# Optimization experiments

Measured on AMD Instinct MI355X. Metric: run time of the kernel, lower is better.

Reference implementation:

```python
import jax, jax.numpy as jnp
import numpy as np

B, T, C, HEAD = 4, 4096, 1024, 64
SCALE = 1.0 / (C ** 0.5)  # module divides by embedding_size**0.5, not head_size**0.5


def setup_inputs() -> dict:
    key = jax.random.key(0)
    kx, kq, kk, kv = jax.random.split(key, 4)
    x = jax.random.normal(kx, (B, T, C), dtype=jnp.float32)
    # nn.Linear(C, head_size, bias=False) weights, stored as (C, head_size) for x @ W
    Wq = jax.random.normal(kq, (C, HEAD), dtype=jnp.float32) * (1.0 / np.sqrt(C))
    Wk = jax.random.normal(kk, (C, HEAD), dtype=jnp.float32) * (1.0 / np.sqrt(C))
    Wv = jax.random.normal(kv, (C, HEAD), dtype=jnp.float32) * (1.0 / np.sqrt(C))
    return {"x": x, "Wq": Wq, "Wk": Wk, "Wv": Wv}


def reference(x, Wq, Wk, Wv):
    q = jnp.einsum('btc,ch->bth', x, Wq)  # [B,T,HEAD]
    k = jnp.einsum('btc,ch->bth', x, Wk)
    v = jnp.einsum('btc,ch->bth', x, Wv)
    aff = jnp.einsum('bqh,bkh->bqk', q, k) * SCALE  # [B,T,T]
    causal = jnp.tril(jnp.ones((T, T), dtype=bool))
    aff = jnp.where(causal, aff, -jnp.inf)
    p = jax.nn.softmax(aff, axis=-1)  # dropout p=0.0 -> identity
    return jnp.einsum('bqk,bkh->bqh', p, v)  # [B,T,HEAD]
```

## Files before the change

kernel.cpp:

```cpp
#include <hip/hip_runtime.h>

#define T_SEQ 4096
#define NBATCH 4
#define CDIM 1024
#define NHEAD 64
#define SCALE (1.0f / 32.0f)
#define LOG2E 1.4426950408889634f
#define BT (NBATCH * T_SEQ)
#define NW 8
#define WREG 8960
#define THR2 11.0f

typedef __bf16 bf16x8 __attribute__((ext_vector_type(8)));
typedef float f32x4 __attribute__((ext_vector_type(4)));
typedef float f32x16 __attribute__((ext_vector_type(16)));
typedef unsigned long long u64;

__device__ __forceinline__ unsigned short f2bf(float f) {
  union { float f; unsigned u; } x;
  x.f = f;
  unsigned r = x.u + 0x7FFFu + ((x.u >> 16) & 1u);
  return (unsigned short)(r >> 16);
}

__device__ __forceinline__ unsigned cvt_pk(float lo, float hi) {
  unsigned d;
  asm("v_cvt_pk_bf16_f32 %0, %1, %2" : "=v"(d) : "v"(lo), "v"(hi));
  return d;
}

__device__ __forceinline__ f32x4 mfma16(bf16x8 a, bf16x8 b, f32x4 c) {
  return __builtin_amdgcn_mfma_f32_16x16x32_bf16(a, b, c, 0, 0, 0);
}

__device__ __forceinline__ f32x16 mfma32(bf16x8 a, bf16x8 b, f32x16 c) {
  return __builtin_amdgcn_mfma_f32_32x32x16_bf16(a, b, c, 0, 0, 0);
}

__global__ void prep_w(const float* __restrict__ Wq, const float* __restrict__ Wk,
                       const float* __restrict__ Wv, unsigned short* __restrict__ Wt) {
  int c = blockIdx.x;
  const float* W = (c < 64) ? Wq : (c < 128) ? Wk : Wv;
  int cc = c & 63;
  float sc = (c < 64) ? (SCALE * LOG2E) : 1.0f;
  for (int k = threadIdx.x; k < CDIM; k += blockDim.x)
    Wt[c * CDIM + k] = f2bf(W[k * NHEAD + cc] * sc);
}

__global__ __launch_bounds__(256) void proj_qkv(
    const float* __restrict__ x, const unsigned short* __restrict__ Wt,
    unsigned short* __restrict__ qws, unsigned short* __restrict__ kws,
    unsigned short* __restrict__ vtws) {
  __shared__ unsigned short xlds[32][136];
  const int tid = threadIdx.x;
  const int lane = tid & 63;
  const int w = tid >> 6;
  const int g = lane >> 4;
  const int c15 = lane & 15;
  const int rb = blockIdx.x * 32;

  f32x4 acc[2][3];
  for (int i = 0; i < 2; i++)
    for (int j = 0; j < 3; j++) acc[i][j] = (f32x4){0.f, 0.f, 0.f, 0.f};

  const int sr = tid >> 3;
  const int scc = (tid & 7) * 16;
  const float* xrow = x + (size_t)(rb + sr) * CDIM + scc;

  float4 cur[4];
  for (int i = 0; i < 4; i++) cur[i] = *(const float4*)(xrow + i * 4);

  for (int k0 = 0; k0 < CDIM; k0 += 128) {
    unsigned short pk[16];
    for (int i = 0; i < 4; i++) {
      pk[i * 4 + 0] = f2bf(cur[i].x);
      pk[i * 4 + 1] = f2bf(cur[i].y);
      pk[i * 4 + 2] = f2bf(cur[i].z);
      pk[i * 4 + 3] = f2bf(cur[i].w);
    }
    *(bf16x8*)&xlds[sr][scc] = *(bf16x8*)&pk[0];
    *(bf16x8*)&xlds[sr][scc + 8] = *(bf16x8*)&pk[8];
    __syncthreads();
    if (k0 + 128 < CDIM)
      for (int i = 0; i < 4; i++)
        cur[i] = *(const float4*)(xrow + k0 + 128 + i * 4);

    bf16x8 wfrag[4][3];
    for (int kk = 0; kk < 4; kk++)
      for (int bn = 0; bn < 3; bn++) {
        int col = w * 48 + bn * 16 + c15;
        wfrag[kk][bn] =
            *(const bf16x8*)&Wt[(size_t)col * CDIM + k0 + kk * 32 + g * 8];
      }

    for (int kk = 0; kk < 4; kk++) {
      bf16x8 a[2];
      for (int mt = 0; mt < 2; mt++)
        a[mt] = *(bf16x8*)&xlds[mt * 16 + c15][kk * 32 + g * 8];
      for (int bn = 0; bn < 3; bn++)
        for (int mt = 0; mt < 2; mt++)
          acc[mt][bn] = mfma16(a[mt], wfrag[kk][bn], acc[mt][bn]);
    }
    __syncthreads();
  }

  for (int mt = 0; mt < 2; mt++)
    for (int bn = 0; bn < 3; bn++) {
      int col = w * 48 + bn * 16 + c15;
      int row0 = rb + mt * 16 + 4 * g;
      for (int r = 0; r < 4; r++) {
        unsigned short v = f2bf(acc[mt][bn][r]);
        int t = row0 + r;
        if (col < 64)
          qws[(size_t)t * 64 + col] = v;
        else if (col < 128)
          kws[(size_t)t * 64 + (col - 64)] = v;
        else
          vtws[(size_t)(col - 128) * BT + t] = v;
      }
    }
}

__global__ __launch_bounds__(512, 2) void attn_fwd(
    const unsigned short* __restrict__ qws, const unsigned short* __restrict__ kws,
    const unsigned short* __restrict__ vtws, float* __restrict__ out) {
  __shared__ __align__(16) char smem[NW * WREG];
  const int tid = threadIdx.x;
  const int lane = tid & 63;
  const int w = tid >> 6;
  const int q31 = lane & 31;
  const int hi = lane >> 5;
  const int b = blockIdx.x >> 6;
  const int pi = blockIdx.x & 63;
  const size_t rowbase = (size_t)b * T_SEQ;
  char* wbase = smem + w * WREG;

  for (int half = 0; half < 2; ++half) {
    const int qt = half ? (127 - pi) : pi;
    const int qb = qt * 32;
    const int nsteps = qt + 1;

    bf16x8 qf[4];
    for (int h2 = 0; h2 < 4; h2++)
      qf[h2] = *(const bf16x8*)&qws[(rowbase + qb + q31) * 64 + h2 * 16 + hi * 8];

    f32x16 o[2];
    o[0] = (f32x16)0.f;
    o[1] = (f32x16)0.f;
    float mrow = -1e30f;
    float lrun = 0.f;

    for (int st = w; st < nsteps; st += NW) {
      const int kt = st * 32;
      bf16x8 ka[4];
      for (int h2 = 0; h2 < 4; h2++)
        ka[h2] =
            *(const bf16x8*)&kws[(rowbase + kt + q31) * 64 + h2 * 16 + hi * 8];
      bf16x8 va[2][2];
      for (int nt = 0; nt < 2; nt++)
        for (int ki = 0; ki < 2; ki++)
          va[nt][ki] = *(const bf16x8*)&vtws[(size_t)(nt * 32 + q31) * BT +
                                             rowbase + kt + ki * 16 + hi * 8];

      f32x16 s = (f32x16)0.f;
      for (int h2 = 0; h2 < 4; h2++) s = mfma32(ka[h2], qf[h2], s);

      float sv[16];
      for (int r = 0; r < 16; r++) sv[r] = s[r];

      if (st == nsteps - 1) {
        for (int r = 0; r < 16; r++) {
          int key = kt + (r & 3) + 8 * (r >> 2) + 4 * hi;
          if (key > qb + q31) sv[r] = -1e30f;
        }
      }

      float t01 = fmaxf(sv[0], sv[1]), t23 = fmaxf(sv[2], sv[3]);
      float t45 = fmaxf(sv[4], sv[5]), t67 = fmaxf(sv[6], sv[7]);
      float t89 = fmaxf(sv[8], sv[9]), tab = fmaxf(sv[10], sv[11]);
      float tcd = fmaxf(sv[12], sv[13]), tef = fmaxf(sv[14], sv[15]);
      float t = fmaxf(fmaxf(fmaxf(t01, t23), fmaxf(t45, t67)),
                      fmaxf(fmaxf(t89, tab), fmaxf(tcd, tef)));
      t = fmaxf(t, __shfl_xor(t, 32));
      if (__any(t > mrow + THR2)) {
        float mn = fmaxf(mrow, t);
        float a = exp2f(mrow - mn);
        mrow = mn;
        o[0] *= a;
        o[1] *= a;
        lrun *= a;
      }
      float p[16];
      for (int r = 0; r < 16; r++) p[r] = exp2f(sv[r] - mrow);

      float ssum = 0.f;
      for (int r = 0; r < 16; r++) ssum += p[r];
      lrun += ssum + __shfl_xor(ssum, 32);

      unsigned X[8], Y[8];
      for (int j = 0; j < 8; j++) X[j] = cvt_pk(p[2 * j], p[2 * j + 1]);
      for (int j = 0; j < 8; j++) Y[j] = __shfl_xor(X[j], 32);

      union { unsigned u[4]; bf16x8 v; } bf0, bf1;
      bf0.u[0] = hi ? Y[2] : X[0];
      bf0.u[1] = hi ? Y[3] : X[1];
      bf0.u[2] = hi ? X[2] : Y[0];
      bf0.u[3] = hi ? X[3] : Y[1];
      bf1.u[0] = hi ? Y[6] : X[4];
      bf1.u[1] = hi ? Y[7] : X[5];
      bf1.u[2] = hi ? X[6] : Y[4];
      bf1.u[3] = hi ? X[7] : Y[5];

      for (int nt = 0; nt < 2; nt++) {
        o[nt] = mfma32(va[nt][0], bf0.v, o[nt]);
        o[nt] = mfma32(va[nt][1], bf1.v, o[nt]);
      }
    }

    float* ow = (float*)wbase;
    float* mw = (float*)(wbase + 8704);
    float* lw = (float*)(wbase + 8832);
    for (int nt = 0; nt < 2; nt++)
      for (int r = 0; r < 16; r++) {
        int d = nt * 32 + (r & 3) + 8 * (r >> 2) + 4 * hi;
        ow[q31 * 68 + d] = o[nt][r];
      }
    if (hi == 0) {
      mw[q31] = mrow;
      lw[q31] = lrun;
    }
    __syncthreads();

    for (int i = 0; i < 4; i++) {
      int e = tid + i * 512;
      int row = e >> 6;
      int d = e & 63;
      float M = -1e30f;
      for (int ww = 0; ww < NW; ww++)
        M = fmaxf(M, ((const float*)(smem + ww * WREG + 8704))[row]);
      float L = 0.f, O = 0.f;
      for (int ww = 0; ww < NW; ww++) {
        float mv = ((const float*)(smem + ww * WREG + 8704))[row];
        float f = exp2f(mv - M);
        L += f * ((const float*)(smem + ww * WREG + 8832))[row];
        O += f * ((const float*)(smem + ww * WREG))[row * 68 + d];
      }
      out[(rowbase + qb + row) * 64 + d] = O / L;
    }
    __syncthreads();
  }
}

extern "C" void kernel_launch(void* const* d_in, const int* in_sizes, int n_in,
                              void* d_out, int out_size, void* d_ws, size_t ws_size,
                              hipStream_t stream) {
  const float* x = (const float*)d_in[0];
  const float* Wq = (const float*)d_in[1];
  const float* Wk = (const float*)d_in[2];
  const float* Wv = (const float*)d_in[3];
  float* out = (float*)d_out;

  char* ws = (char*)d_ws;
  unsigned short* Wt = (unsigned short*)(ws);
  unsigned short* qws = (unsigned short*)(ws + 393216);
  unsigned short* kws = (unsigned short*)(ws + 393216 + 2097152);
  unsigned short* vtws = (unsigned short*)(ws + 393216 + 2 * 2097152);

  prep_w<<<dim3(192), dim3(256), 0, stream>>>(Wq, Wk, Wv, Wt);
  proj_qkv<<<dim3(512), dim3(256), 0, stream>>>(x, Wt, qws, kws, vtws);
  attn_fwd<<<dim3(256), dim3(512), 0, stream>>>(qws, kws, vtws, out);
}
```

Measured before the change: 79.65 us.

## Double-buffer projection LDS, use permlane32 swap, drop lazy rescale

The QKV projection kernel gains a second LDS buffer, so the next x tile is converted and stored while the current one is consumed by MFMAs, which removes one barrier per k-step. In the attention loop, eight cross-half shuffles plus selects are replaced with four v_permlane32_swap instructions to build the P operand. The thresholded lazy max rescale is also dropped in favour of an unconditional rescale every step. That removes the wave-wide vote and branch, but adds an exp2 and multiplies of the O accumulators on every step.

```diff
diff --git a/kernel.cpp b/kernel.cpp
--- a/kernel.cpp
+++ b/kernel.cpp
@@ -9,12 +9,10 @@
 #define BT (NBATCH * T_SEQ)
 #define NW 8
 #define WREG 8960
-#define THR2 11.0f
 
 typedef __bf16 bf16x8 __attribute__((ext_vector_type(8)));
 typedef float f32x4 __attribute__((ext_vector_type(4)));
 typedef float f32x16 __attribute__((ext_vector_type(16)));
-typedef unsigned long long u64;
 
 __device__ __forceinline__ unsigned short f2bf(float f) {
   union { float f; unsigned u; } x;
@@ -27,6 +25,10 @@
   unsigned d;
   asm("v_cvt_pk_bf16_f32 %0, %1, %2" : "=v"(d) : "v"(lo), "v"(hi));
   return d;
+}
+
+__device__ __forceinline__ void swap32(unsigned& a, unsigned& b) {
+  asm("v_permlane32_swap_b32 %0, %1" : "+v"(a), "+v"(b));
 }
 
 __device__ __forceinline__ f32x4 mfma16(bf16x8 a, bf16x8 b, f32x4 c) {
@@ -51,7 +53,7 @@
     const float* __restrict__ x, const unsigned short* __restrict__ Wt,
     unsigned short* __restrict__ qws, unsigned short* __restrict__ kws,
     unsigned short* __restrict__ vtws) {
-  __shared__ unsigned short xlds[32][136];
+  __shared__ unsigned short xlds[2][32][136];
   const int tid = threadIdx.x;
   const int lane = tid & 63;
   const int w = tid >> 6;
@@ -67,10 +69,9 @@
   const int scc = (tid & 7) * 16;
   const float* xrow = x + (size_t)(rb + sr) * CDIM + scc;
 
-  float4 cur[4];
-  for (int i = 0; i < 4; i++) cur[i] = *(const float4*)(xrow + i * 4);
-
-  for (int k0 = 0; k0 < CDIM; k0 += 128) {
+  {
+    float4 cur[4];
+    for (int i = 0; i < 4; i++) cur[i] = *(const float4*)(xrow + i * 4);
     unsigned short pk[16];
     for (int i = 0; i < 4; i++) {
       pk[i * 4 + 0] = f2bf(cur[i].x);
@@ -78,12 +79,18 @@
       pk[i * 4 + 2] = f2bf(cur[i].z);
       pk[i * 4 + 3] = f2bf(cur[i].w);
     }
-    *(bf16x8*)&xlds[sr][scc] = *(bf16x8*)&pk[0];
-    *(bf16x8*)&xlds[sr][scc + 8] = *(bf16x8*)&pk[8];
-    __syncthreads();
-    if (k0 + 128 < CDIM)
+    *(bf16x8*)&xlds[0][sr][scc] = *(bf16x8*)&pk[0];
+    *(bf16x8*)&xlds[0][sr][scc + 8] = *(bf16x8*)&pk[8];
+  }
+  __syncthreads();
+
+  int pb = 0;
+  for (int k0 = 0; k0 < CDIM; k0 += 128) {
+    const bool more = (k0 + 128 < CDIM);
+    float4 nxt[4];
+    if (more)
       for (int i = 0; i < 4; i++)
-        cur[i] = *(const float4*)(xrow + k0 + 128 + i * 4);
+        nxt[i] = *(const float4*)(xrow + k0 + 128 + i * 4);
 
     bf16x8 wfrag[4][3];
     for (int kk = 0; kk < 4; kk++)
@@ -96,12 +103,25 @@
     for (int kk = 0; kk < 4; kk++) {
       bf16x8 a[2];
       for (int mt = 0; mt < 2; mt++)
-        a[mt] = *(bf16x8*)&xlds[mt * 16 + c15][kk * 32 + g * 8];
+        a[mt] = *(bf16x8*)&xlds[pb][mt * 16 + c15][kk * 32 + g * 8];
       for (int bn = 0; bn < 3; bn++)
         for (int mt = 0; mt < 2; mt++)
           acc[mt][bn] = mfma16(a[mt], wfrag[kk][bn], acc[mt][bn]);
     }
+
+    if (more) {
+      unsigned short pk[16];
+      for (int i = 0; i < 4; i++) {
+        pk[i * 4 + 0] = f2bf(nxt[i].x);
+        pk[i * 4 + 1] = f2bf(nxt[i].y);
+        pk[i * 4 + 2] = f2bf(nxt[i].z);
+        pk[i * 4 + 3] = f2bf(nxt[i].w);
+      }
+      *(bf16x8*)&xlds[pb ^ 1][sr][scc] = *(bf16x8*)&pk[0];
+      *(bf16x8*)&xlds[pb ^ 1][sr][scc + 8] = *(bf16x8*)&pk[8];
+    }
     __syncthreads();
+    pb ^= 1;
   }
 
   for (int mt = 0; mt < 2; mt++)
@@ -182,14 +202,14 @@
       float t = fmaxf(fmaxf(fmaxf(t01, t23), fmaxf(t45, t67)),
                       fmaxf(fmaxf(t89, tab), fmaxf(tcd, tef)));
       t = fmaxf(t, __shfl_xor(t, 32));
-      if (__any(t > mrow + THR2)) {
-        float mn = fmaxf(mrow, t);
-        float a = exp2f(mrow - mn);
-        mrow = mn;
-        o[0] *= a;
-        o[1] *= a;
-        lrun *= a;
-      }
+
+      float mn = fmaxf(mrow, t);
+      float a = exp2f(mrow - mn);
+      mrow = mn;
+      o[0] *= a;
+      o[1] *= a;
+      lrun *= a;
+
       float p[16];
       for (int r = 0; r < 16; r++) p[r] = exp2f(sv[r] - mrow);
 
@@ -197,19 +217,16 @@
       for (int r = 0; r < 16; r++) ssum += p[r];
       lrun += ssum + __shfl_xor(ssum, 32);
 
-      unsigned X[8], Y[8];
-      for (int j = 0; j < 8; j++) X[j] = cvt_pk(p[2 * j], p[2 * j + 1]);
-      for (int j = 0; j < 8; j++) Y[j] = __shfl_xor(X[j], 32);
+      unsigned X[8];
+      for (int jj = 0; jj < 8; jj++) X[jj] = cvt_pk(p[2 * jj], p[2 * jj + 1]);
+      swap32(X[0], X[2]);
+      swap32(X[1], X[3]);
+      swap32(X[4], X[6]);
+      swap32(X[5], X[7]);
 
       union { unsigned u[4]; bf16x8 v; } bf0, bf1;
-      bf0.u[0] = hi ? Y[2] : X[0];
-      bf0.u[1] = hi ? Y[3] : X[1];
-      bf0.u[2] = hi ? X[2] : Y[0];
-      bf0.u[3] = hi ? X[3] : Y[1];
-      bf1.u[0] = hi ? Y[6] : X[4];
-      bf1.u[1] = hi ? Y[7] : X[5];
-      bf1.u[2] = hi ? X[6] : Y[4];
-      bf1.u[3] = hi ? X[7] : Y[5];
+      bf0.u[0] = X[0]; bf0.u[1] = X[1]; bf0.u[2] = X[2]; bf0.u[3] = X[3];
+      bf1.u[0] = X[4]; bf1.u[1] = X[5]; bf1.u[2] = X[6]; bf1.u[3] = X[7];
 
       for (int nt = 0; nt < 2; nt++) {
         o[nt] = mfma32(va[nt][0], bf0.v, o[nt]);
```

New measurement: 79.79 us. Within noise of the previous version (+0.2%).
